# Kernel optimization log

Measured on AMD Instinct MI355X. Metric: run time of the kernel, lower is better.

## Reference

```python
import jax, jax.numpy as jnp
import numpy as np

C = 512
B, W, H = 16, 64, 64
K = 128


def setup_inputs() -> dict:
    key = jax.random.key(0)
    ks = jax.random.split(key, 17)
    s = 0.02
    inp = {
        "x1": jax.random.normal(ks[0], (B, C, W, H), jnp.float32),
        "y1": jax.random.normal(ks[1], (B, K, C), jnp.float32),
        "x2": jax.random.normal(ks[2], (B, C, W, H), jnp.float32),
        "y2": jax.random.normal(ks[3], (B, K, C), jnp.float32),
        # 1x1 conv weights stored as [out, in]
        "wq1": jax.random.normal(ks[4], (C // 4, C), jnp.float32) * s,
        "bq1": jnp.zeros((C // 4,), jnp.float32),
        "wq2": jax.random.normal(ks[5], (C // 4, C), jnp.float32) * s,
        "bq2": jnp.zeros((C // 4,), jnp.float32),
        "wk1": jax.random.normal(ks[6], (C // 2, C), jnp.float32) * s,
        "bk1": jnp.zeros((C // 2,), jnp.float32),
        "wk2": jax.random.normal(ks[7], (C // 2, C), jnp.float32) * s,
        "bk2": jnp.zeros((C // 2,), jnp.float32),
        "wv1": jax.random.normal(ks[8], (C, C), jnp.float32) * s,
        "bv1": jnp.zeros((C,), jnp.float32),
        "wv2": jax.random.normal(ks[9], (C, C), jnp.float32) * s,
        "bv2": jnp.zeros((C,), jnp.float32),
        "scale": jnp.ones((1,), jnp.float32) * 0.5,  # nn.Parameter(zeros) would kill grads; nonzero for testing
    }
    return inp


def reference(x1, y1, x2, y2, wq1, bq1, wq2, bq2, wk1, bk1, wk2, bk2,
              wv1, bv1, wv2, bv2, scale):
    b, c, w, h = x1.shape
    n = w * h
    # 1x1 convs == channel-wise linear maps
    q1 = jnp.einsum('bcwh,dc->bdwh', x1, wq1) + bq1[None, :, None, None]
    q2 = jnp.einsum('bcwh,dc->bdwh', x2, wq2) + bq2[None, :, None, None]
    # concat along channels -> [B, C/2, N] -> [B, N, C/2]
    q = jnp.concatenate([q1, q2], axis=1).reshape(b, c // 2, n).transpose(0, 2, 1)
    k1 = y1 @ wk1.T + bk1  # [B, K, C/2]
    k2 = y2 @ wk2.T + bk2
    v1 = y1 @ wv1.T + bv1  # [B, K, C]
    v2 = y2 @ wv2.T + bv2
    e1 = jnp.einsum('bnd,bkd->bnk', q, k1)  # [B, N, K]
    e2 = jnp.einsum('bnd,bkd->bnk', q, k2)
    attn = jax.nn.softmax(jnp.abs(e1 - e2), axis=-1)
    # out = value^T @ attn^T : [B, C, N]
    o1 = jnp.einsum('bkc,bnk->bcn', v1, attn).reshape(b, c, w, h)
    o2 = jnp.einsum('bkc,bnk->bcn', v2, attn).reshape(b, c, w, h)
    out1 = scale[0] * o1 + x1
    out2 = scale[0] * o2 + x2
    return out1, out2
```

## Files before the change

kernel.cpp:

```cpp
#include <hip/hip_runtime.h>

typedef unsigned short u16;
typedef __attribute__((ext_vector_type(8))) short short8v;
typedef __attribute__((ext_vector_type(4))) float floatx4;

#define B_ 16
#define C_ 512
#define N_ 4096
#define K_ 128
#define NT 64

__device__ __forceinline__ float bf2f(u16 u) {
    unsigned int x = ((unsigned int)u) << 16;
    return __builtin_bit_cast(float, x);
}
__device__ __forceinline__ u16 f2bf(float f) {
    unsigned int u = __builtin_bit_cast(unsigned int, f);
    u = u + 0x7FFFu + ((u >> 16) & 1u);
    return (u16)(u >> 16);
}

__global__ void conv_all(const float* __restrict__ y1, const float* __restrict__ y2,
                         const float* __restrict__ wk1, const float* __restrict__ wk2,
                         const float* __restrict__ wv1, const float* __restrict__ wv2,
                         u16* y1b, u16* y2b, u16* wk1b, u16* wk2b, u16* wv1b, u16* wv2b) {
    int tid = blockIdx.x * 256 + threadIdx.x;
    const int SY = B_ * K_ * C_;
    const int SWK = 256 * 512;
    const int SWV = 512 * 512;
    const float* src; u16* dst; int off;
    if (tid < SY)                 { src = y1;  dst = y1b;  off = tid; }
    else if (tid < 2*SY)          { src = y2;  dst = y2b;  off = tid - SY; }
    else if (tid < 2*SY+SWK)      { src = wk1; dst = wk1b; off = tid - 2*SY; }
    else if (tid < 2*SY+2*SWK)    { src = wk2; dst = wk2b; off = tid - 2*SY - SWK; }
    else if (tid < 2*SY+2*SWK+SWV){ src = wv1; dst = wv1b; off = tid - 2*SY - 2*SWK; }
    else                          { src = wv2; dst = wv2b; off = tid - 2*SY - 2*SWK - SWV; }
    dst[off] = f2bf(src[off]);
}

__global__ void conv_wqt(const float* __restrict__ wq1, const float* __restrict__ wq2,
                         u16* wq1t, u16* wq2t) {
    int tid = blockIdx.x * 256 + threadIdx.x;
    const float* s = (tid & 65536) ? wq2 : wq1;
    u16* d = (tid & 65536) ? wq2t : wq1t;
    int e = tid & 65535;
    int dd = e >> 9;
    int c = e & 511;
    d[c * 128 + dd] = f2bf(s[dd * 512 + c]);
}

__global__ void gemm_gk(const u16* __restrict__ y1b, const u16* __restrict__ y2b,
                        const u16* __restrict__ wk1b, const u16* __restrict__ wk2b,
                        const float* __restrict__ bk1, const float* __restrict__ bk2,
                        u16* k1b, u16* k2b) {
    int l = threadIdx.x;
    int z = blockIdx.z; int b = z >> 1; int which = z & 1;
    const u16* A = (which ? y2b : y1b) + (size_t)b * K_ * C_;
    const u16* Wt = which ? wk2b : wk1b;
    const float* bias = which ? bk2 : bk1;
    u16* outp = (which ? k2b : k1b) + (size_t)b * K_ * 256;
    int m0 = blockIdx.x * 64, n0 = blockIdx.y * 64;
    floatx4 acc[4][4] = {};
    for (int ch = 0; ch < 16; ++ch) {
        int koff = ch * 32 + (l >> 4) * 8;
        short8v a[4], wv[4];
#pragma unroll
        for (int mf = 0; mf < 4; ++mf) a[mf] = *(const short8v*)(A + (size_t)(m0 + mf*16 + (l & 15)) * 512 + koff);
#pragma unroll
        for (int nf = 0; nf < 4; ++nf) wv[nf] = *(const short8v*)(Wt + (size_t)(n0 + nf*16 + (l & 15)) * 512 + koff);
#pragma unroll
        for (int mf = 0; mf < 4; ++mf)
#pragma unroll
            for (int nf = 0; nf < 4; ++nf)
                acc[mf][nf] = __builtin_amdgcn_mfma_f32_16x16x32_bf16(a[mf], wv[nf], acc[mf][nf], 0, 0, 0);
    }
#pragma unroll
    for (int mf = 0; mf < 4; ++mf)
#pragma unroll
        for (int nf = 0; nf < 4; ++nf)
#pragma unroll
            for (int rg = 0; rg < 4; ++rg) {
                int m = m0 + mf*16 + (l >> 4)*4 + rg;
                int n = n0 + nf*16 + (l & 15);
                outp[(size_t)m * 256 + n] = f2bf(acc[mf][nf][rg] + bias[n]);
            }
}

__global__ void ebias_k(const u16* __restrict__ k1b, const u16* __restrict__ k2b,
                        const float* __restrict__ bq1, const float* __restrict__ bq2,
                        float* eb1, float* eb2) {
    int tid = blockIdx.x * 256 + threadIdx.x;
    int pair = tid >> 11; int inner = tid & 2047;
    int b = inner >> 7; int key = inner & 127;
    const u16* kb = (pair ? k2b : k1b) + ((size_t)(b * 128 + key)) * 256;
    float s = 0.f;
    for (int d = 0; d < 128; ++d) s += bq1[d] * bf2f(kb[d]);
    for (int d = 0; d < 128; ++d) s += bq2[d] * bf2f(kb[128 + d]);
    (pair ? eb2 : eb1)[b * 128 + key] = s;
}

__global__ void gemm_gkk(const u16* __restrict__ k1b, const u16* __restrict__ k2b,
                         const u16* __restrict__ wq1t, const u16* __restrict__ wq2t,
                         u16* kk11, u16* kk12, u16* kk21, u16* kk22) {
    int l = threadIdx.x;
    int z = blockIdx.z; int b = z >> 2; int which = z & 3;
    const u16* A = ((which < 2) ? k1b : k2b) + (size_t)b * K_ * 256 + (which & 1) * 128;
    const u16* Wt = (which & 1) ? wq2t : wq1t;
    u16* outp;
    switch (which) { case 0: outp = kk11; break; case 1: outp = kk12; break;
                     case 2: outp = kk21; break; default: outp = kk22; }
    outp += (size_t)b * K_ * C_;
    int m0 = blockIdx.x * 64, n0 = blockIdx.y * 64;
    floatx4 acc[4][4] = {};
    for (int ch = 0; ch < 4; ++ch) {
        int koff = ch * 32 + (l >> 4) * 8;
        short8v a[4], wv[4];
#pragma unroll
        for (int mf = 0; mf < 4; ++mf) a[mf] = *(const short8v*)(A + (size_t)(m0 + mf*16 + (l & 15)) * 256 + koff);
#pragma unroll
        for (int nf = 0; nf < 4; ++nf) wv[nf] = *(const short8v*)(Wt + (size_t)(n0 + nf*16 + (l & 15)) * 128 + koff);
#pragma unroll
        for (int mf = 0; mf < 4; ++mf)
#pragma unroll
            for (int nf = 0; nf < 4; ++nf)
                acc[mf][nf] = __builtin_amdgcn_mfma_f32_16x16x32_bf16(a[mf], wv[nf], acc[mf][nf], 0, 0, 0);
    }
#pragma unroll
    for (int mf = 0; mf < 4; ++mf)
#pragma unroll
        for (int nf = 0; nf < 4; ++nf)
#pragma unroll
            for (int rg = 0; rg < 4; ++rg) {
                int m = m0 + mf*16 + (l >> 4)*4 + rg;
                int n = n0 + nf*16 + (l & 15);
                outp[(size_t)m * C_ + n] = f2bf(acc[mf][nf][rg]);
            }
}

__global__ void gemm_gv(const u16* __restrict__ wv1b, const u16* __restrict__ wv2b,
                        const u16* __restrict__ y1b, const u16* __restrict__ y2b,
                        const float* __restrict__ bv1, const float* __restrict__ bv2,
                        u16* vt1, u16* vt2) {
    int l = threadIdx.x;
    int z = blockIdx.z; int b = z >> 1; int which = z & 1;
    const u16* A = which ? wv2b : wv1b;
    const u16* Wt = (which ? y2b : y1b) + (size_t)b * K_ * C_;
    const float* bias = which ? bv2 : bv1;
    u16* outp = (which ? vt2 : vt1) + (size_t)b * C_ * K_;
    int m0 = blockIdx.x * 64, n0 = blockIdx.y * 64;
    floatx4 acc[4][4] = {};
    for (int ch = 0; ch < 16; ++ch) {
        int koff = ch * 32 + (l >> 4) * 8;
        short8v a[4], wv[4];
#pragma unroll
        for (int mf = 0; mf < 4; ++mf) a[mf] = *(const short8v*)(A + (size_t)(m0 + mf*16 + (l & 15)) * 512 + koff);
#pragma unroll
        for (int nf = 0; nf < 4; ++nf) wv[nf] = *(const short8v*)(Wt + (size_t)(n0 + nf*16 + (l & 15)) * 512 + koff);
#pragma unroll
        for (int mf = 0; mf < 4; ++mf)
#pragma unroll
            for (int nf = 0; nf < 4; ++nf)
                acc[mf][nf] = __builtin_amdgcn_mfma_f32_16x16x32_bf16(a[mf], wv[nf], acc[mf][nf], 0, 0, 0);
    }
#pragma unroll
    for (int mf = 0; mf < 4; ++mf)
#pragma unroll
        for (int nf = 0; nf < 4; ++nf)
#pragma unroll
            for (int rg = 0; rg < 4; ++rg) {
                int m = m0 + mf*16 + (l >> 4)*4 + rg;
                int n = n0 + nf*16 + (l & 15);
                outp[(size_t)m * K_ + n] = f2bf(acc[mf][nf][rg] + bias[m]);
            }
}

__global__ __launch_bounds__(256, 2)
void main_attn(const float* __restrict__ x1, const float* __restrict__ x2,
               const u16* __restrict__ kk11, const u16* __restrict__ kk12,
               const u16* __restrict__ kk21, const u16* __restrict__ kk22,
               const u16* __restrict__ vt1, const u16* __restrict__ vt2,
               const float* __restrict__ eb1, const float* __restrict__ eb2,
               const float* __restrict__ scale_p,
               float* __restrict__ out1, float* __restrict__ out2) {
    __shared__ u16 regionA[20480];
    __shared__ u16 attn_s[64 * 128];

    u16* xT = regionA;
    u16* kk1s = regionA + 4096;
    u16* kk2s = regionA + 4096 + 8192;
    float* s_f = (float*)regionA;
    float* red1 = (float*)regionA + 64 * 132;
    float* red2 = red1 + 256;

    int bid0 = blockIdx.x;
    int bid = ((bid0 & 7) << 7) | (bid0 >> 3);
    int b = bid >> 6;
    int n0 = (bid & 63) * NT;
    int t = threadIdx.x;
    int w = t >> 6;
    int l = t & 63;

    const float sc = scale_p[0];

    floatx4 e1a[4][2] = {}; floatx4 e2a[4][2] = {};

    const float* xs0 = x1 + (size_t)b * C_ * N_;
    const float* xs1 = x2 + (size_t)b * C_ * N_;
    const u16* kkAh[2] = { kk11 + (size_t)b * K_ * C_, kk12 + (size_t)b * K_ * C_ };
    const u16* kkBh[2] = { kk21 + (size_t)b * K_ * C_, kk22 + (size_t)b * K_ * C_ };

    for (int r = 0; r < 16; ++r) {
        int half = r >> 3;
        int c0 = (r & 7) * 64;
        {
            const float* xp = (half ? xs1 : xs0) + (size_t)(c0 + w * 16 + (l >> 5) * 8) * N_ + n0 + 2 * (l & 31);
            float v0[8], v1[8];
#pragma unroll
            for (int j = 0; j < 8; ++j) { float2 f = *(const float2*)(xp + (size_t)j * N_); v0[j] = f.x; v1[j] = f.y; }
            short8v p0, p1;
#pragma unroll
            for (int j = 0; j < 8; ++j) { p0[j] = (short)f2bf(v0[j]); p1[j] = (short)f2bf(v1[j]); }
            int row0 = 2 * (l & 31), row1 = row0 + 1;
            int g = w * 2 + (l >> 5);
            *(short8v*)&xT[row0 * 64 + 8 * (g ^ (row0 & 7))] = p0;
            *(short8v*)&xT[row1 * 64 + 8 * (g ^ (row1 & 7))] = p1;
        }
        {
            int key = w * 32 + (l >> 1);
            const u16* s1 = kkAh[half] + (size_t)key * C_ + c0;
            const u16* s2 = kkBh[half] + (size_t)key * C_ + c0;
#pragma unroll
            for (int i = 0; i < 4; ++i) {
                int g = (l & 1) * 4 + i;
                short8v q1 = *(const short8v*)(s1 + g * 8);
                short8v q2 = *(const short8v*)(s2 + g * 8);
                int didx = key * 64 + 8 * (g ^ (key & 7));
                *(short8v*)&kk1s[didx] = q1;
                *(short8v*)&kk2s[didx] = q2;
            }
        }
        __syncthreads();
#pragma unroll
        for (int ch = 0; ch < 2; ++ch) {
            short8v a[4];
#pragma unroll
            for (int mf = 0; mf < 4; ++mf) {
                int row = mf * 16 + (l & 15);
                int g = ch * 4 + (l >> 4);
                a[mf] = *(const short8v*)&xT[row * 64 + 8 * (g ^ (row & 7))];
            }
#pragma unroll
            for (int kf = 0; kf < 2; ++kf) {
                int krow = w * 32 + kf * 16 + (l & 15);
                int g = ch * 4 + (l >> 4);
                int idx = krow * 64 + 8 * (g ^ (krow & 7));
                short8v b1 = *(const short8v*)&kk1s[idx];
                short8v b2 = *(const short8v*)&kk2s[idx];
#pragma unroll
                for (int mf = 0; mf < 4; ++mf) {
                    e1a[mf][kf] = __builtin_amdgcn_mfma_f32_16x16x32_bf16(a[mf], b1, e1a[mf][kf], 0, 0, 0);
                    e2a[mf][kf] = __builtin_amdgcn_mfma_f32_16x16x32_bf16(a[mf], b2, e2a[mf][kf], 0, 0, 0);
                }
            }
        }
        __syncthreads();
    }

    float ebv1[2], ebv2[2];
#pragma unroll
    for (int kf = 0; kf < 2; ++kf) {
        int kc = w * 32 + kf * 16 + (l & 15);
        ebv1[kf] = eb1[b * 128 + kc];
        ebv2[kf] = eb2[b * 128 + kc];
    }
#pragma unroll
    for (int mf = 0; mf < 4; ++mf)
#pragma unroll
        for (int kf = 0; kf < 2; ++kf)
#pragma unroll
            for (int rg = 0; rg < 4; ++rg) {
                int row = mf * 16 + (l >> 4) * 4 + rg;
                int col = w * 32 + kf * 16 + (l & 15);
                s_f[row * 132 + col] = fabsf(e1a[mf][kf][rg] + ebv1[kf] - e2a[mf][kf][rg] - ebv2[kf]);
            }
    __syncthreads();
    {
        int rrow = l; int q = w;
        float m = -1e30f;
        for (int i = 0; i < 32; ++i) m = fmaxf(m, s_f[rrow * 132 + q * 32 + i]);
        red1[q * 64 + rrow] = m;
        __syncthreads();
        float mrow = fmaxf(fmaxf(red1[rrow], red1[64 + rrow]), fmaxf(red1[128 + rrow], red1[192 + rrow]));
        float ps = 0.f;
        for (int i = 0; i < 32; ++i) {
            float e = __expf(s_f[rrow * 132 + q * 32 + i] - mrow);
            s_f[rrow * 132 + q * 32 + i] = e;
            ps += e;
        }
        red2[q * 64 + rrow] = ps;
        __syncthreads();
        float inv = 1.0f / (red2[rrow] + red2[64 + rrow] + red2[128 + rrow] + red2[192 + rrow]);
#pragma unroll
        for (int g2 = 0; g2 < 4; ++g2) {
            int g = q * 4 + g2;
            short8v pk;
#pragma unroll
            for (int j = 0; j < 8; ++j) pk[j] = (short)f2bf(s_f[rrow * 132 + g * 8 + j] * inv);
            *(short8v*)&attn_s[rrow * 128 + 8 * (g ^ (rrow & 7))] = pk;
        }
    }
    __syncthreads();

    for (int oi = 0; oi < 2; ++oi) {
        const u16* vt = (oi ? vt2 : vt1) + (size_t)b * C_ * K_;
        const float* xr = oi ? xs1 : xs0;
        float* op = (oi ? out2 : out1) + (size_t)b * C_ * N_;
        for (int cc = 0; cc < 4; ++cc) {
            {
                int rowl = t >> 1;
                const u16* vs = vt + (size_t)(cc * 128 + rowl) * K_;
#pragma unroll
                for (int i = 0; i < 8; ++i) {
                    int g = (t & 1) * 8 + i;
                    short8v q0 = *(const short8v*)(vs + g * 8);
                    *(short8v*)&regionA[rowl * 128 + 8 * (g ^ (rowl & 7))] = q0;
                }
            }
            __syncthreads();
            floatx4 o[2][4] = {};
#pragma unroll
            for (int kc = 0; kc < 4; ++kc) {
                short8v a[2];
#pragma unroll
                for (int mf = 0; mf < 2; ++mf) {
                    int row = w * 32 + mf * 16 + (l & 15);
                    int g = kc * 4 + (l >> 4);
                    a[mf] = *(const short8v*)&regionA[row * 128 + 8 * (g ^ (row & 7))];
                }
#pragma unroll
                for (int nf = 0; nf < 4; ++nf) {
                    int nrow = nf * 16 + (l & 15);
                    int g = kc * 4 + (l >> 4);
                    short8v bb = *(const short8v*)&attn_s[nrow * 128 + 8 * (g ^ (nrow & 7))];
#pragma unroll
                    for (int mf = 0; mf < 2; ++mf)
                        o[mf][nf] = __builtin_amdgcn_mfma_f32_16x16x32_bf16(a[mf], bb, o[mf][nf], 0, 0, 0);
                }
            }
#pragma unroll
            for (int mf = 0; mf < 2; ++mf)
#pragma unroll
                for (int nf = 0; nf < 4; ++nf)
#pragma unroll
                    for (int rg = 0; rg < 4; ++rg) {
                        int c = cc * 128 + w * 32 + mf * 16 + (l >> 4) * 4 + rg;
                        int n = n0 + nf * 16 + (l & 15);
                        size_t idx = (size_t)c * N_ + n;
                        op[idx] = sc * o[mf][nf][rg] + xr[idx];
                    }
            __syncthreads();
        }
    }
}

extern "C" void kernel_launch(void* const* d_in, const int* in_sizes, int n_in,
                              void* d_out, int out_size, void* d_ws, size_t ws_size,
                              hipStream_t stream) {
    const float* x1 = (const float*)d_in[0];
    const float* y1 = (const float*)d_in[1];
    const float* x2 = (const float*)d_in[2];
    const float* y2 = (const float*)d_in[3];
    const float* wq1 = (const float*)d_in[4];
    const float* bq1 = (const float*)d_in[5];
    const float* wq2 = (const float*)d_in[6];
    const float* bq2 = (const float*)d_in[7];
    const float* wk1 = (const float*)d_in[8];
    const float* bk1 = (const float*)d_in[9];
    const float* wk2 = (const float*)d_in[10];
    const float* bk2 = (const float*)d_in[11];
    const float* wv1 = (const float*)d_in[12];
    const float* bv1 = (const float*)d_in[13];
    const float* wv2 = (const float*)d_in[14];
    const float* bv2 = (const float*)d_in[15];
    const float* scale = (const float*)d_in[16];

    char* ws = (char*)d_ws;
    u16* y1b  = (u16*)(ws + 0);
    u16* y2b  = (u16*)(ws + 2097152);
    u16* wk1b = (u16*)(ws + 4194304);
    u16* wk2b = (u16*)(ws + 4456448);
    u16* wv1b = (u16*)(ws + 4718592);
    u16* wv2b = (u16*)(ws + 5242880);
    u16* wq1t = (u16*)(ws + 5767168);
    u16* wq2t = (u16*)(ws + 5898240);
    u16* k1b  = (u16*)(ws + 6029312);
    u16* k2b  = (u16*)(ws + 7077888);
    u16* kk11 = (u16*)(ws + 8126464);
    u16* kk12 = (u16*)(ws + 10223616);
    u16* kk21 = (u16*)(ws + 12320768);
    u16* kk22 = (u16*)(ws + 14417920);
    u16* vt1  = (u16*)(ws + 16515072);
    u16* vt2  = (u16*)(ws + 18612224);
    float* eb1 = (float*)(ws + 20709376);
    float* eb2 = (float*)(ws + 20717568);

    float* out1 = (float*)d_out;
    float* out2 = out1 + (size_t)B_ * C_ * N_;

    hipLaunchKernelGGL(conv_all, dim3(11264), dim3(256), 0, stream,
                       y1, y2, wk1, wk2, wv1, wv2, y1b, y2b, wk1b, wk2b, wv1b, wv2b);
    hipLaunchKernelGGL(conv_wqt, dim3(512), dim3(256), 0, stream, wq1, wq2, wq1t, wq2t);
    hipLaunchKernelGGL(gemm_gk, dim3(2, 4, 32), dim3(64), 0, stream,
                       y1b, y2b, wk1b, wk2b, bk1, bk2, k1b, k2b);
    hipLaunchKernelGGL(ebias_k, dim3(16), dim3(256), 0, stream, k1b, k2b, bq1, bq2, eb1, eb2);
    hipLaunchKernelGGL(gemm_gkk, dim3(2, 8, 64), dim3(64), 0, stream,
                       k1b, k2b, wq1t, wq2t, kk11, kk12, kk21, kk22);
    hipLaunchKernelGGL(gemm_gv, dim3(8, 2, 32), dim3(64), 0, stream,
                       wv1b, wv2b, y1b, y2b, bv1, bv2, vt1, vt2);
    hipLaunchKernelGGL(main_attn, dim3(1024), dim3(256), 0, stream,
                       x1, x2, kk11, kk12, kk21, kk22, vt1, vt2, eb1, eb2, scale,
                       out1, out2);
}
```

Baseline: 260.0 us.

## Merge prep kernels, prefetch x tiles, read kk/vt directly from global in attention

Folds the wq transpose conversion into conv_all and merges the key and value projection GEMMs into one launch, cutting launch count. In main_attn, the next x tile is prefetched into registers while the current tile is computed. kk and vt operands are read straight from global/L2 instead of being staged through LDS, which drops several barriers. That frees shared memory, so the score buffer pitch shrinks and launch bounds go from 2 to 3 blocks per SM. The trade-off is uncoalesced direct global loads and more register pressure, with a risk of spills under the tighter occupancy target.

```diff
diff --git a/kernel.cpp b/kernel.cpp
--- a/kernel.cpp
+++ b/kernel.cpp
@@ -23,43 +23,63 @@
 __global__ void conv_all(const float* __restrict__ y1, const float* __restrict__ y2,
                          const float* __restrict__ wk1, const float* __restrict__ wk2,
                          const float* __restrict__ wv1, const float* __restrict__ wv2,
-                         u16* y1b, u16* y2b, u16* wk1b, u16* wk2b, u16* wv1b, u16* wv2b) {
+                         const float* __restrict__ wq1, const float* __restrict__ wq2,
+                         u16* y1b, u16* y2b, u16* wk1b, u16* wk2b, u16* wv1b, u16* wv2b,
+                         u16* wq1t, u16* wq2t) {
     int tid = blockIdx.x * 256 + threadIdx.x;
     const int SY = B_ * K_ * C_;
     const int SWK = 256 * 512;
     const int SWV = 512 * 512;
-    const float* src; u16* dst; int off;
-    if (tid < SY)                 { src = y1;  dst = y1b;  off = tid; }
-    else if (tid < 2*SY)          { src = y2;  dst = y2b;  off = tid - SY; }
-    else if (tid < 2*SY+SWK)      { src = wk1; dst = wk1b; off = tid - 2*SY; }
-    else if (tid < 2*SY+2*SWK)    { src = wk2; dst = wk2b; off = tid - 2*SY - SWK; }
-    else if (tid < 2*SY+2*SWK+SWV){ src = wv1; dst = wv1b; off = tid - 2*SY - 2*SWK; }
-    else                          { src = wv2; dst = wv2b; off = tid - 2*SY - 2*SWK - SWV; }
-    dst[off] = f2bf(src[off]);
-}
-
-__global__ void conv_wqt(const float* __restrict__ wq1, const float* __restrict__ wq2,
-                         u16* wq1t, u16* wq2t) {
-    int tid = blockIdx.x * 256 + threadIdx.x;
-    const float* s = (tid & 65536) ? wq2 : wq1;
-    u16* d = (tid & 65536) ? wq2t : wq1t;
-    int e = tid & 65535;
-    int dd = e >> 9;
-    int c = e & 511;
-    d[c * 128 + dd] = f2bf(s[dd * 512 + c]);
-}
-
-__global__ void gemm_gk(const u16* __restrict__ y1b, const u16* __restrict__ y2b,
-                        const u16* __restrict__ wk1b, const u16* __restrict__ wk2b,
-                        const float* __restrict__ bk1, const float* __restrict__ bk2,
-                        u16* k1b, u16* k2b) {
+    const int SQ = 128 * 512;
+    int base = 2*SY + 2*SWK + 2*SWV;
+    if (tid < base) {
+        const float* src; u16* dst; int off;
+        if (tid < SY)                 { src = y1;  dst = y1b;  off = tid; }
+        else if (tid < 2*SY)          { src = y2;  dst = y2b;  off = tid - SY; }
+        else if (tid < 2*SY+SWK)      { src = wk1; dst = wk1b; off = tid - 2*SY; }
+        else if (tid < 2*SY+2*SWK)    { src = wk2; dst = wk2b; off = tid - 2*SY - SWK; }
+        else if (tid < 2*SY+2*SWK+SWV){ src = wv1; dst = wv1b; off = tid - 2*SY - 2*SWK; }
+        else                          { src = wv2; dst = wv2b; off = tid - 2*SY - 2*SWK - SWV; }
+        dst[off] = f2bf(src[off]);
+    } else {
+        int e = tid - base;
+        const float* s = (e >= SQ) ? wq2 : wq1;
+        u16* d = (e >= SQ) ? wq2t : wq1t;
+        e &= (SQ - 1);
+        int dd = e >> 9;
+        int c = e & 511;
+        d[c * 128 + dd] = f2bf(s[dd * 512 + c]);
+    }
+}
+
+__global__ void gemm_gkgv(const u16* __restrict__ y1b, const u16* __restrict__ y2b,
+                          const u16* __restrict__ wk1b, const u16* __restrict__ wk2b,
+                          const u16* __restrict__ wv1b, const u16* __restrict__ wv2b,
+                          const float* __restrict__ bk1, const float* __restrict__ bk2,
+                          const float* __restrict__ bv1, const float* __restrict__ bv2,
+                          u16* k1b, u16* k2b, u16* vt1, u16* vt2) {
     int l = threadIdx.x;
-    int z = blockIdx.z; int b = z >> 1; int which = z & 1;
-    const u16* A = (which ? y2b : y1b) + (size_t)b * K_ * C_;
-    const u16* Wt = which ? wk2b : wk1b;
-    const float* bias = which ? bk2 : bk1;
-    u16* outp = (which ? k2b : k1b) + (size_t)b * K_ * 256;
-    int m0 = blockIdx.x * 64, n0 = blockIdx.y * 64;
+    int id = blockIdx.x;
+    const u16 *A, *Bt; const float* bias; u16* outp;
+    int m0, n0, po; bool bias_m;
+    if (id < 256) {
+        int bx = id & 1, by = (id >> 1) & 3, z = id >> 3;
+        int b = z >> 1, which = z & 1;
+        A = (which ? y2b : y1b) + (size_t)b * K_ * C_;
+        Bt = which ? wk2b : wk1b;
+        bias = which ? bk2 : bk1;
+        outp = (which ? k2b : k1b) + (size_t)b * K_ * 256;
+        m0 = bx * 64; n0 = by * 64; po = 256; bias_m = false;
+    } else {
+        int id2 = id - 256;
+        int bx = id2 & 7, by = (id2 >> 3) & 1, z = id2 >> 4;
+        int b = z >> 1, which = z & 1;
+        A = which ? wv2b : wv1b;
+        Bt = (which ? y2b : y1b) + (size_t)b * K_ * C_;
+        bias = which ? bv2 : bv1;
+        outp = (which ? vt2 : vt1) + (size_t)b * C_ * K_;
+        m0 = bx * 64; n0 = by * 64; po = 128; bias_m = true;
+    }
     floatx4 acc[4][4] = {};
     for (int ch = 0; ch < 16; ++ch) {
         int koff = ch * 32 + (l >> 4) * 8;
@@ -67,7 +87,7 @@
 #pragma unroll
         for (int mf = 0; mf < 4; ++mf) a[mf] = *(const short8v*)(A + (size_t)(m0 + mf*16 + (l & 15)) * 512 + koff);
 #pragma unroll
-        for (int nf = 0; nf < 4; ++nf) wv[nf] = *(const short8v*)(Wt + (size_t)(n0 + nf*16 + (l & 15)) * 512 + koff);
+        for (int nf = 0; nf < 4; ++nf) wv[nf] = *(const short8v*)(Bt + (size_t)(n0 + nf*16 + (l & 15)) * 512 + koff);
 #pragma unroll
         for (int mf = 0; mf < 4; ++mf)
 #pragma unroll
@@ -82,7 +102,7 @@
             for (int rg = 0; rg < 4; ++rg) {
                 int m = m0 + mf*16 + (l >> 4)*4 + rg;
                 int n = n0 + nf*16 + (l & 15);
-                outp[(size_t)m * 256 + n] = f2bf(acc[mf][nf][rg] + bias[n]);
+                outp[(size_t)m * po + n] = f2bf(acc[mf][nf][rg] + (bias_m ? bias[m] : bias[n]));
             }
 }
 
@@ -137,44 +157,7 @@
             }
 }
 
-__global__ void gemm_gv(const u16* __restrict__ wv1b, const u16* __restrict__ wv2b,
-                        const u16* __restrict__ y1b, const u16* __restrict__ y2b,
-                        const float* __restrict__ bv1, const float* __restrict__ bv2,
-                        u16* vt1, u16* vt2) {
-    int l = threadIdx.x;
-    int z = blockIdx.z; int b = z >> 1; int which = z & 1;
-    const u16* A = which ? wv2b : wv1b;
-    const u16* Wt = (which ? y2b : y1b) + (size_t)b * K_ * C_;
-    const float* bias = which ? bv2 : bv1;
-    u16* outp = (which ? vt2 : vt1) + (size_t)b * C_ * K_;
-    int m0 = blockIdx.x * 64, n0 = blockIdx.y * 64;
-    floatx4 acc[4][4] = {};
-    for (int ch = 0; ch < 16; ++ch) {
-        int koff = ch * 32 + (l >> 4) * 8;
-        short8v a[4], wv[4];
-#pragma unroll
-        for (int mf = 0; mf < 4; ++mf) a[mf] = *(const short8v*)(A + (size_t)(m0 + mf*16 + (l & 15)) * 512 + koff);
-#pragma unroll
-        for (int nf = 0; nf < 4; ++nf) wv[nf] = *(const short8v*)(Wt + (size_t)(n0 + nf*16 + (l & 15)) * 512 + koff);
-#pragma unroll
-        for (int mf = 0; mf < 4; ++mf)
-#pragma unroll
-            for (int nf = 0; nf < 4; ++nf)
-                acc[mf][nf] = __builtin_amdgcn_mfma_f32_16x16x32_bf16(a[mf], wv[nf], acc[mf][nf], 0, 0, 0);
-    }
-#pragma unroll
-    for (int mf = 0; mf < 4; ++mf)
-#pragma unroll
-        for (int nf = 0; nf < 4; ++nf)
-#pragma unroll
-            for (int rg = 0; rg < 4; ++rg) {
-                int m = m0 + mf*16 + (l >> 4)*4 + rg;
-                int n = n0 + nf*16 + (l & 15);
-                outp[(size_t)m * K_ + n] = f2bf(acc[mf][nf][rg] + bias[m]);
-            }
-}
-
-__global__ __launch_bounds__(256, 2)
+__global__ __launch_bounds__(256, 3)
 void main_attn(const float* __restrict__ x1, const float* __restrict__ x2,
                const u16* __restrict__ kk11, const u16* __restrict__ kk12,
                const u16* __restrict__ kk21, const u16* __restrict__ kk22,
@@ -182,14 +165,12 @@
                const float* __restrict__ eb1, const float* __restrict__ eb2,
                const float* __restrict__ scale_p,
                float* __restrict__ out1, float* __restrict__ out2) {
-    __shared__ u16 regionA[20480];
+    __shared__ float regionF[8768];
     __shared__ u16 attn_s[64 * 128];
 
-    u16* xT = regionA;
-    u16* kk1s = regionA + 4096;
-    u16* kk2s = regionA + 4096 + 8192;
-    float* s_f = (float*)regionA;
-    float* red1 = (float*)regionA + 64 * 132;
+    u16* xT = (u16*)regionF;
+    float* s_f = regionF;
+    float* red1 = regionF + 64 * 129;
     float* red2 = red1 + 256;
 
     int bid0 = blockIdx.x;
@@ -206,40 +187,39 @@
 
     const float* xs0 = x1 + (size_t)b * C_ * N_;
     const float* xs1 = x2 + (size_t)b * C_ * N_;
-    const u16* kkAh[2] = { kk11 + (size_t)b * K_ * C_, kk12 + (size_t)b * K_ * C_ };
-    const u16* kkBh[2] = { kk21 + (size_t)b * K_ * C_, kk22 + (size_t)b * K_ * C_ };
-
-    for (int r = 0; r < 16; ++r) {
+    const u16* kk11p = kk11 + (size_t)b * K_ * C_;
+    const u16* kk12p = kk12 + (size_t)b * K_ * C_;
+    const u16* kk21p = kk21 + (size_t)b * K_ * C_;
+    const u16* kk22p = kk22 + (size_t)b * K_ * C_;
+
+    float pv0[8], pv1[8];
+    auto load_x = [&](int r) {
         int half = r >> 3;
         int c0 = (r & 7) * 64;
+        const float* xp = (half ? xs1 : xs0) + (size_t)(c0 + w * 16 + (l >> 5) * 8) * N_ + n0 + 2 * (l & 31);
+#pragma unroll
+        for (int j = 0; j < 8; ++j) { float2 f = *(const float2*)(xp + (size_t)j * N_); pv0[j] = f.x; pv1[j] = f.y; }
+    };
+
+    load_x(0);
+    for (int r = 0; r < 16; ++r) {
+        if (r) __syncthreads();
         {
-            const float* xp = (half ? xs1 : xs0) + (size_t)(c0 + w * 16 + (l >> 5) * 8) * N_ + n0 + 2 * (l & 31);
-            float v0[8], v1[8];
-#pragma unroll
-            for (int j = 0; j < 8; ++j) { float2 f = *(const float2*)(xp + (size_t)j * N_); v0[j] = f.x; v1[j] = f.y; }
             short8v p0, p1;
 #pragma unroll
-            for (int j = 0; j < 8; ++j) { p0[j] = (short)f2bf(v0[j]); p1[j] = (short)f2bf(v1[j]); }
+            for (int j = 0; j < 8; ++j) { p0[j] = (short)f2bf(pv0[j]); p1[j] = (short)f2bf(pv1[j]); }
             int row0 = 2 * (l & 31), row1 = row0 + 1;
             int g = w * 2 + (l >> 5);
             *(short8v*)&xT[row0 * 64 + 8 * (g ^ (row0 & 7))] = p0;
             *(short8v*)&xT[row1 * 64 + 8 * (g ^ (row1 & 7))] = p1;
         }
-        {
-            int key = w * 32 + (l >> 1);
-            const u16* s1 = kkAh[half] + (size_t)key * C_ + c0;
-            const u16* s2 = kkBh[half] + (size_t)key * C_ + c0;
-#pragma unroll
-            for (int i = 0; i < 4; ++i) {
-                int g = (l & 1) * 4 + i;
-                short8v q1 = *(const short8v*)(s1 + g * 8);
-                short8v q2 = *(const short8v*)(s2 + g * 8);
-                int didx = key * 64 + 8 * (g ^ (key & 7));
-                *(short8v*)&kk1s[didx] = q1;
-                *(short8v*)&kk2s[didx] = q2;
-            }
-        }
         __syncthreads();
+        if (r < 15) load_x(r + 1);
+
+        int half = r >> 3;
+        int c0 = (r & 7) * 64;
+        const u16* kkA = half ? kk12p : kk11p;
+        const u16* kkB = half ? kk22p : kk21p;
 #pragma unroll
         for (int ch = 0; ch < 2; ++ch) {
             short8v a[4];
@@ -251,11 +231,9 @@
             }
 #pragma unroll
             for (int kf = 0; kf < 2; ++kf) {
-                int krow = w * 32 + kf * 16 + (l & 15);
-                int g = ch * 4 + (l >> 4);
-                int idx = krow * 64 + 8 * (g ^ (krow & 7));
-                short8v b1 = *(const short8v*)&kk1s[idx];
-                short8v b2 = *(const short8v*)&kk2s[idx];
+                size_t off = (size_t)(w * 32 + kf * 16 + (l & 15)) * 512 + c0 + ch * 32 + (l >> 4) * 8;
+                short8v b1 = *(const short8v*)(kkA + off);
+                short8v b2 = *(const short8v*)(kkB + off);
 #pragma unroll
                 for (int mf = 0; mf < 4; ++mf) {
                     e1a[mf][kf] = __builtin_amdgcn_mfma_f32_16x16x32_bf16(a[mf], b1, e1a[mf][kf], 0, 0, 0);
@@ -263,8 +241,8 @@
                 }
             }
         }
-        __syncthreads();
-    }
+    }
+    __syncthreads();
 
     float ebv1[2], ebv2[2];
 #pragma unroll
@@ -281,20 +259,20 @@
             for (int rg = 0; rg < 4; ++rg) {
                 int row = mf * 16 + (l >> 4) * 4 + rg;
                 int col = w * 32 + kf * 16 + (l & 15);
-                s_f[row * 132 + col] = fabsf(e1a[mf][kf][rg] + ebv1[kf] - e2a[mf][kf][rg] - ebv2[kf]);
+                s_f[row * 129 + col] = fabsf(e1a[mf][kf][rg] + ebv1[kf] - e2a[mf][kf][rg] - ebv2[kf]);
             }
     __syncthreads();
     {
         int rrow = l; int q = w;
         float m = -1e30f;
-        for (int i = 0; i < 32; ++i) m = fmaxf(m, s_f[rrow * 132 + q * 32 + i]);
+        for (int i = 0; i < 32; ++i) m = fmaxf(m, s_f[rrow * 129 + q * 32 + i]);
         red1[q * 64 + rrow] = m;
         __syncthreads();
         float mrow = fmaxf(fmaxf(red1[rrow], red1[64 + rrow]), fmaxf(red1[128 + rrow], red1[192 + rrow]));
         float ps = 0.f;
         for (int i = 0; i < 32; ++i) {
-            float e = __expf(s_f[rrow * 132 + q * 32 + i] - mrow);
-            s_f[rrow * 132 + q * 32 + i] = e;
+            float e = __expf(s_f[rrow * 129 + q * 32 + i] - mrow);
+            s_f[rrow * 129 + q * 32 + i] = e;
             ps += e;
         }
         red2[q * 64 + rrow] = ps;
@@ -305,7 +283,7 @@
             int g = q * 4 + g2;
             short8v pk;
 #pragma unroll
-            for (int j = 0; j < 8; ++j) pk[j] = (short)f2bf(s_f[rrow * 132 + g * 8 + j] * inv);
+            for (int j = 0; j < 8; ++j) pk[j] = (short)f2bf(s_f[rrow * 129 + g * 8 + j] * inv);
             *(short8v*)&attn_s[rrow * 128 + 8 * (g ^ (rrow & 7))] = pk;
         }
     }
@@ -315,27 +293,16 @@
         const u16* vt = (oi ? vt2 : vt1) + (size_t)b * C_ * K_;
         const float* xr = oi ? xs1 : xs0;
         float* op = (oi ? out2 : out1) + (size_t)b * C_ * N_;
+#pragma unroll
         for (int cc = 0; cc < 4; ++cc) {
-            {
-                int rowl = t >> 1;
-                const u16* vs = vt + (size_t)(cc * 128 + rowl) * K_;
-#pragma unroll
-                for (int i = 0; i < 8; ++i) {
-                    int g = (t & 1) * 8 + i;
-                    short8v q0 = *(const short8v*)(vs + g * 8);
-                    *(short8v*)&regionA[rowl * 128 + 8 * (g ^ (rowl & 7))] = q0;
-                }
-            }
-            __syncthreads();
             floatx4 o[2][4] = {};
 #pragma unroll
             for (int kc = 0; kc < 4; ++kc) {
                 short8v a[2];
 #pragma unroll
                 for (int mf = 0; mf < 2; ++mf) {
-                    int row = w * 32 + mf * 16 + (l & 15);
-                    int g = kc * 4 + (l >> 4);
-                    a[mf] = *(const short8v*)&regionA[row * 128 + 8 * (g ^ (row & 7))];
+                    size_t row = cc * 128 + w * 32 + mf * 16 + (l & 15);
+                    a[mf] = *(const short8v*)(vt + row * K_ + kc * 32 + (l >> 4) * 8);
                 }
 #pragma unroll
                 for (int nf = 0; nf < 4; ++nf) {
@@ -358,7 +325,6 @@
                         size_t idx = (size_t)c * N_ + n;
                         op[idx] = sc * o[mf][nf][rg] + xr[idx];
                     }
-            __syncthreads();
         }
     }
 }
@@ -407,16 +373,15 @@
     float* out1 = (float*)d_out;
     float* out2 = out1 + (size_t)B_ * C_ * N_;
 
-    hipLaunchKernelGGL(conv_all, dim3(11264), dim3(256), 0, stream,
-                       y1, y2, wk1, wk2, wv1, wv2, y1b, y2b, wk1b, wk2b, wv1b, wv2b);
-    hipLaunchKernelGGL(conv_wqt, dim3(512), dim3(256), 0, stream, wq1, wq2, wq1t, wq2t);
-    hipLaunchKernelGGL(gemm_gk, dim3(2, 4, 32), dim3(64), 0, stream,
-                       y1b, y2b, wk1b, wk2b, bk1, bk2, k1b, k2b);
+    hipLaunchKernelGGL(conv_all, dim3(11776), dim3(256), 0, stream,
+                       y1, y2, wk1, wk2, wv1, wv2, wq1, wq2,
+                       y1b, y2b, wk1b, wk2b, wv1b, wv2b, wq1t, wq2t);
+    hipLaunchKernelGGL(gemm_gkgv, dim3(768), dim3(64), 0, stream,
+                       y1b, y2b, wk1b, wk2b, wv1b, wv2b, bk1, bk2, bv1, bv2,
+                       k1b, k2b, vt1, vt2);
     hipLaunchKernelGGL(ebias_k, dim3(16), dim3(256), 0, stream, k1b, k2b, bq1, bq2, eb1, eb2);
     hipLaunchKernelGGL(gemm_gkk, dim3(2, 8, 64), dim3(64), 0, stream,
                        k1b, k2b, wq1t, wq2t, kk11, kk12, kk21, kk22);
-    hipLaunchKernelGGL(gemm_gv, dim3(8, 2, 32), dim3(64), 0, stream,
-                       wv1b, wv2b, y1b, y2b, bv1, bv2, vt1, vt2);
     hipLaunchKernelGGL(main_attn, dim3(1024), dim3(256), 0, stream,
                        x1, x2, kk11, kk12, kk21, kk22, vt1, vt2, eb1, eb2, scale,
                        out1, out2);
```

Result: slower. 541.7 us (+108.3%).
